# Performance work log

Measured on AMD Instinct MI355X. Metric: run time of the kernel, lower is better.

The kernel has to match this reference:

```python
import jax, jax.numpy as jnp
import numpy as np

LAMB = 0.5  # penalty coefficient (init kwarg lamb)


def setup_inputs() -> dict:
    key = jax.random.key(0)
    k1, k2, k3 = jax.random.split(key, 3)
    B, T, D, K = 4, 512, 256, 512
    reps = jax.random.normal(k1, (B, T, D), jnp.float32)
    rep_table = jax.random.normal(k2, (B, T, T, D), jnp.float32)
    centers = jax.random.normal(k3, (K, D), jnp.float32)
    return {"reps": reps, "rep_table": rep_table, "centers": centers, "timestep": T}


def reference(reps, rep_table, centers, timestep):
    B, T, D = reps.shape
    t = timestep  # min(max_len, timestep) with max_len=1e9
    dtype = reps.dtype

    # ~mask after torch.flip: row i keeps columns j >= t-1-i  (segment length i+1)
    keep = (jnp.arange(t)[None, :] >= (t - 1 - jnp.arange(t))[:, None]).astype(dtype)
    seg_lengths = jnp.arange(t, dtype=dtype) + 1.0  # (t,)

    # masked segment sum over dim 2, then average: (B, t, D)
    x = jnp.einsum('ij,bijd->bid', keep, rep_table[:, :t, :t]) / seg_lengths[None, :, None]

    # codebook attention: softmax(x C^T / sqrt(D)) C  -> (B, t, D)
    scale = 1.0 / jnp.sqrt(jnp.asarray(D, dtype))
    attn = jax.nn.softmax(jnp.einsum('bid,kd->bik', x, centers) * scale, axis=-1)
    xa = jnp.einsum('bik,kd->bid', attn, centers)

    # L2 distance to each center, expanded form to avoid (B,t,K,D) tensor
    l2 = (jnp.sum(xa * xa, axis=-1)[:, :, None]
          - 2.0 * jnp.einsum('bid,kd->bik', xa, centers)
          + jnp.sum(centers * centers, axis=-1)[None, None, :])  # (B, t, K)

    loss = l2 + (LAMB * (1.0 - seg_lengths))[None, :, None]

    val = jnp.min(loss, axis=2)      # (B, t)
    idxs = jnp.argmin(loss, axis=2)  # (B, t)

    costs = jnp.full((B, T + 1), jnp.inf, dtype).at[:, :t].set(val[:, ::-1])
    tokens = jnp.zeros((B, T + 1), jnp.int32).at[:, :t].set(idxs[:, ::-1].astype(jnp.int32))
    return costs, tokens
```

## Files before the change

kernel.cpp:

```cpp
#include <hip/hip_runtime.h>
#include <math.h>
#include <float.h>

#define TT 512
#define DD 256
#define KK 512
#define LAMBDA 0.5f

typedef float f4 __attribute__((ext_vector_type(4)));

__device__ __forceinline__ f4 ntload(const f4* p) {
    return __builtin_nontemporal_load(p);
}

__device__ __forceinline__ void fma4(f4& a, float s, f4 c) {
    a.x = fmaf(s, c.x, a.x);
    a.y = fmaf(s, c.y, a.y);
    a.z = fmaf(s, c.z, a.z);
    a.w = fmaf(s, c.w, a.w);
}

__device__ __forceinline__ unsigned short f2bf(float f) {
    unsigned int u = __float_as_uint(f);
    unsigned int r = (u + 0x7FFFu + ((u >> 16) & 1u)) >> 16;
    return (unsigned short)r;
}

__global__ __launch_bounds__(256) void seg_mean_kernel(const float* __restrict__ tbl,
                                                       float* __restrict__ x) {
    const int blk = blockIdx.x;
    const int b = blk >> 8;
    const int p = blk & 255;
    const int i0 = p;
    const int i1 = TT - 1 - p;
    const int tid = threadIdx.x;
    const int jj = tid >> 6;
    const int d4 = tid & 63;

    const f4* __restrict__ base0 =
        (const f4*)tbl + (size_t)(b * TT + i0) * (TT * (DD / 4));
    const f4* __restrict__ base1 =
        (const f4*)tbl + (size_t)(b * TT + i1) * (TT * (DD / 4));

    f4 accA = (f4)(0.f), accB = (f4)(0.f);
    {
        int j = TT - 1 - p + jj;
        for (; j + 4 < TT; j += 8) {
            f4 v0 = ntload(base0 + (size_t)j * 64 + d4);
            f4 v1 = ntload(base0 + (size_t)(j + 4) * 64 + d4);
            accA += v0; accB += v1;
        }
        if (j < TT) accA += ntload(base0 + (size_t)j * 64 + d4);
    }
    f4 acc0 = accA + accB;
    accA = (f4)(0.f); accB = (f4)(0.f);
    {
        int j = p + jj;
        for (; j + 4 < TT; j += 8) {
            f4 v0 = ntload(base1 + (size_t)j * 64 + d4);
            f4 v1 = ntload(base1 + (size_t)(j + 4) * 64 + d4);
            accA += v0; accB += v1;
        }
        if (j < TT) accA += ntload(base1 + (size_t)j * 64 + d4);
    }
    f4 acc1 = accA + accB;

    __shared__ f4 red0[4][64];
    __shared__ f4 red1[4][64];
    red0[jj][d4] = acc0;
    red1[jj][d4] = acc1;
    __syncthreads();
    if (tid < 128) {
        const int r = tid >> 6;
        const int d = tid & 63;
        const f4 (*red)[64] = r ? red1 : red0;
        const int i = r ? i1 : i0;
        f4 o = (red[0][d] + red[1][d]) + (red[2][d] + red[3][d]);
        o *= 0.0625f / (float)(i + 1);
        ((f4*)(x + (size_t)(b * TT + i) * DD))[d] = o;
    }
}

__global__ __launch_bounds__(256) void prep_kernel(const float* __restrict__ C,
                                                   float* __restrict__ CT,
                                                   float* __restrict__ cn2) {
    const int blk = blockIdx.x;
    const int tid = threadIdx.x;
    if (blk < 32) {
        __shared__ float tile[64][65];
        const int k0 = (blk & 7) * 64;
        const int d0 = (blk >> 3) * 64;
        const int kk = tid >> 4;
        const int dl = (tid & 15) * 4;
#pragma unroll
        for (int r = 0; r < 4; ++r) {
            const float4 v = *(const float4*)&C[(size_t)(k0 + kk + r * 16) * DD + d0 + dl];
            tile[kk + r * 16][dl + 0] = v.x;
            tile[kk + r * 16][dl + 1] = v.y;
            tile[kk + r * 16][dl + 2] = v.z;
            tile[kk + r * 16][dl + 3] = v.w;
        }
        __syncthreads();
        const int dd = tid >> 4;
        const int kl = (tid & 15) * 4;
#pragma unroll
        for (int r = 0; r < 4; ++r) {
            const int d = dd + r * 16;
            float4 o = make_float4(tile[kl + 0][d], tile[kl + 1][d],
                                   tile[kl + 2][d], tile[kl + 3][d]);
            *(float4*)&CT[(size_t)(d0 + d) * KK + k0 + kl] = o;
        }
    } else {
        const int w = tid >> 6, lane = tid & 63;
        const int k = (blk - 32) * 4 + w;
        const float4 v = *(const float4*)&C[(size_t)k * DD + lane * 4];
        float s = v.x * v.x + v.y * v.y + v.z * v.z + v.w * v.w;
#pragma unroll
        for (int off = 32; off > 0; off >>= 1) s += __shfl_xor(s, off, 64);
        if (lane == 0) cn2[k] = s;
    }
}

__global__ __launch_bounds__(512) void attn_argmin_kernel(
        const float* __restrict__ x, const float* __restrict__ C,
        const float* __restrict__ CT, const float* __restrict__ cn2,
        unsigned short* __restrict__ out, int Btot) {
    __shared__ char part_raw[65536];
    f4 (*scpart)[8][128] = (f4 (*)[8][128])part_raw;
    f4 (*xpart)[8][64]   = (f4 (*)[8][64])part_raw;
    __shared__ float xs[8][DD];
    __shared__ float sc[8][KK];
    __shared__ float xav[8][DD];
    __shared__ float rinv[8];
    __shared__ float xn2s[8];

    const int tid = threadIdx.x;
    const int lane = tid & 63;
    const int wv = tid >> 6;
    const int row0 = blockIdx.x * 8;

    ((f4*)&xs[0][0])[tid] = ((const f4*)(x + (size_t)row0 * DD))[tid];
    __syncthreads();

    {
        const int g = tid >> 7;
        const int k4 = tid & 127;
        const f4* CTv = (const f4*)CT + (size_t)(g * 64) * (KK / 4) + k4;
        f4 acc[8];
#pragma unroll
        for (int r = 0; r < 8; ++r) acc[r] = (f4)(0.f);
        for (int dd = 0; dd < 64; ++dd) {
            f4 c = CTv[dd * (KK / 4)];
            const int d = g * 64 + dd;
#pragma unroll
            for (int r = 0; r < 8; ++r) fma4(acc[r], xs[r][d], c);
        }
#pragma unroll
        for (int r = 0; r < 8; ++r) scpart[g][r][k4] = acc[r];
    }
    __syncthreads();
    {
#pragma unroll
        for (int it = 0; it < 2; ++it) {
            const int idx = tid * 2 + it;
            const int row = idx >> 7, k4 = idx & 127;
            f4 s = (scpart[0][row][k4] + scpart[1][row][k4])
                 + (scpart[2][row][k4] + scpart[3][row][k4]);
            ((f4*)sc[row])[k4] = s;
        }
    }
    __syncthreads();

    {
        const int r = wv;
        float v[8];
        float m = -INFINITY;
#pragma unroll
        for (int q = 0; q < 8; ++q) {
            v[q] = sc[r][lane + 64 * q];
            m = fmaxf(m, v[q]);
        }
#pragma unroll
        for (int off = 32; off > 0; off >>= 1) m = fmaxf(m, __shfl_xor(m, off, 64));
        float ssum = 0.f;
#pragma unroll
        for (int q = 0; q < 8; ++q) {
            float e = expf(v[q] - m);
            sc[r][lane + 64 * q] = e;
            ssum += e;
        }
#pragma unroll
        for (int off = 32; off > 0; off >>= 1) ssum += __shfl_xor(ssum, off, 64);
        if (lane == 0) rinv[r] = 1.f / ssum;
    }
    __syncthreads();

    {
        const int kb = wv * 64;
        const f4* Cv = (const f4*)C + (size_t)kb * (DD / 4) + lane;
        f4 acc[8];
#pragma unroll
        for (int r = 0; r < 8; ++r) acc[r] = (f4)(0.f);
        for (int kk = 0; kk < 64; ++kk) {
            f4 c = Cv[kk * (DD / 4)];
            const int k = kb + kk;
#pragma unroll
            for (int r = 0; r < 8; ++r) fma4(acc[r], sc[r][k], c);
        }
#pragma unroll
        for (int r = 0; r < 8; ++r) xpart[wv][r][lane] = acc[r];
    }
    __syncthreads();
    {
        const int row = wv, d4 = lane;
        f4 s = ((xpart[0][row][d4] + xpart[1][row][d4])
              + (xpart[2][row][d4] + xpart[3][row][d4]))
             + ((xpart[4][row][d4] + xpart[5][row][d4])
              + (xpart[6][row][d4] + xpart[7][row][d4]));
        s *= rinv[row];
        ((f4*)xav[row])[d4] = s;
        float n = s.x * s.x + s.y * s.y + s.z * s.z + s.w * s.w;
#pragma unroll
        for (int off = 32; off > 0; off >>= 1) n += __shfl_xor(n, off, 64);
        if (lane == 0) xn2s[row] = n;
    }
    __syncthreads();

    {
        const int g = tid >> 7;
        const int k4 = tid & 127;
        const f4* CTv = (const f4*)CT + (size_t)(g * 64) * (KK / 4) + k4;
        f4 acc[8];
#pragma unroll
        for (int r = 0; r < 8; ++r) acc[r] = (f4)(0.f);
        for (int dd = 0; dd < 64; ++dd) {
            f4 c = CTv[dd * (KK / 4)];
            const int d = g * 64 + dd;
#pragma unroll
            for (int r = 0; r < 8; ++r) fma4(acc[r], xav[r][d], c);
        }
#pragma unroll
        for (int r = 0; r < 8; ++r) scpart[g][r][k4] = acc[r];
    }
    __syncthreads();
    {
        float mv = FLT_MAX;
        int mi = 0;
#pragma unroll
        for (int it = 0; it < 2; ++it) {
            const int idx = tid * 2 + it;
            const int k4 = idx & 127;
            f4 dot = (scpart[0][wv][k4] + scpart[1][wv][k4])
                   + (scpart[2][wv][k4] + scpart[3][wv][k4]);
            f4 cn = ((const f4*)cn2)[k4];
            float l0 = cn.x - 2.f * dot.x;
            float l1 = cn.y - 2.f * dot.y;
            float l2 = cn.z - 2.f * dot.z;
            float l3 = cn.w - 2.f * dot.w;
            float lv = l0; int li = k4 * 4;
            if (l1 < lv) { lv = l1; li = k4 * 4 + 1; }
            if (l2 < lv) { lv = l2; li = k4 * 4 + 2; }
            if (l3 < lv) { lv = l3; li = k4 * 4 + 3; }
            if (lv < mv || (lv == mv && li < mi)) { mv = lv; mi = li; }
        }
#pragma unroll
        for (int off = 32; off > 0; off >>= 1) {
            float ov = __shfl_xor(mv, off, 64);
            int oi = __shfl_xor(mi, off, 64);
            if (ov < mv || (ov == mv && oi < mi)) { mv = ov; mi = oi; }
        }
        if (lane == 0) {
            const int row = row0 + wv;
            const int b = row >> 9;
            const int i = row & (TT - 1);
            const float pen = LAMBDA * (1.f - (float)(i + 1));
            const float val = mv + xn2s[wv] + pen;
            out[b * (TT + 1) + (TT - 1 - i)] = f2bf(val);
            out[Btot * (TT + 1) + b * (TT + 1) + (TT - 1 - i)] = f2bf((float)mi);
        }
    }
    if (tid == 511 && (row0 & (TT - 1)) == 0) {
        const int b = row0 >> 9;
        out[b * (TT + 1) + TT] = 0x7F7F;
        out[Btot * (TT + 1) + b * (TT + 1) + TT] = 0;
    }
}

extern "C" void kernel_launch(void* const* d_in, const int* in_sizes, int n_in,
                              void* d_out, int out_size, void* d_ws, size_t ws_size,
                              hipStream_t stream) {
    const float* rep_table = (const float*)d_in[1];
    const float* centers   = (const float*)d_in[2];
    unsigned short* out = (unsigned short*)d_out;

    const int Btot = in_sizes[0] / (TT * DD);

    float* x   = (float*)d_ws;
    float* CT  = x + (size_t)Btot * TT * DD;
    float* cn2 = CT + (size_t)DD * KK;

    prep_kernel<<<160, 256, 0, stream>>>(centers, CT, cn2);
    seg_mean_kernel<<<Btot * (TT / 2), 256, 0, stream>>>(rep_table, x);
    attn_argmin_kernel<<<(Btot * TT) / 8, 512, 0, stream>>>(x, centers, CT, cn2,
                                                            out, Btot);
}
```

Baseline: 113.0 us.

## Merge prep and segment-mean kernels, deepen load unroll, vectorize LDS operand reads

Folds the centers transpose/norm prep into the segment-mean launch as extra blocks, which removes one kernel launch and lets the small prep work overlap the bandwidth-bound table reduction. The segment-sum loop now keeps four independent accumulators with four loads in flight instead of two. The three small matmul loops in the attention kernel read four LDS scalars at once as one f4 and issue four global loads per step, cutting LDS instruction count. Block index ranges are hardcoded for B=4 (1024 segment blocks), so other batch sizes would break.

```diff
diff --git a/kernel.cpp b/kernel.cpp
--- a/kernel.cpp
+++ b/kernel.cpp
@@ -26,70 +26,72 @@
     return (unsigned short)r;
 }
 
-__global__ __launch_bounds__(256) void seg_mean_kernel(const float* __restrict__ tbl,
-                                                       float* __restrict__ x) {
-    const int blk = blockIdx.x;
-    const int b = blk >> 8;
-    const int p = blk & 255;
-    const int i0 = p;
-    const int i1 = TT - 1 - p;
-    const int tid = threadIdx.x;
-    const int jj = tid >> 6;
-    const int d4 = tid & 63;
-
-    const f4* __restrict__ base0 =
-        (const f4*)tbl + (size_t)(b * TT + i0) * (TT * (DD / 4));
-    const f4* __restrict__ base1 =
-        (const f4*)tbl + (size_t)(b * TT + i1) * (TT * (DD / 4));
-
-    f4 accA = (f4)(0.f), accB = (f4)(0.f);
-    {
-        int j = TT - 1 - p + jj;
-        for (; j + 4 < TT; j += 8) {
-            f4 v0 = ntload(base0 + (size_t)j * 64 + d4);
-            f4 v1 = ntload(base0 + (size_t)(j + 4) * 64 + d4);
-            accA += v0; accB += v1;
-        }
-        if (j < TT) accA += ntload(base0 + (size_t)j * 64 + d4);
-    }
-    f4 acc0 = accA + accB;
-    accA = (f4)(0.f); accB = (f4)(0.f);
-    {
-        int j = p + jj;
-        for (; j + 4 < TT; j += 8) {
-            f4 v0 = ntload(base1 + (size_t)j * 64 + d4);
-            f4 v1 = ntload(base1 + (size_t)(j + 4) * 64 + d4);
-            accA += v0; accB += v1;
-        }
-        if (j < TT) accA += ntload(base1 + (size_t)j * 64 + d4);
-    }
-    f4 acc1 = accA + accB;
-
-    __shared__ f4 red0[4][64];
-    __shared__ f4 red1[4][64];
-    red0[jj][d4] = acc0;
-    red1[jj][d4] = acc1;
-    __syncthreads();
-    if (tid < 128) {
-        const int r = tid >> 6;
-        const int d = tid & 63;
-        const f4 (*red)[64] = r ? red1 : red0;
-        const int i = r ? i1 : i0;
-        f4 o = (red[0][d] + red[1][d]) + (red[2][d] + red[3][d]);
-        o *= 0.0625f / (float)(i + 1);
-        ((f4*)(x + (size_t)(b * TT + i) * DD))[d] = o;
-    }
-}
-
-__global__ __launch_bounds__(256) void prep_kernel(const float* __restrict__ C,
-                                                   float* __restrict__ CT,
-                                                   float* __restrict__ cn2) {
+__global__ __launch_bounds__(256) void combo_kernel(
+        const float* __restrict__ tbl, const float* __restrict__ C,
+        float* __restrict__ x, float* __restrict__ CT,
+        float* __restrict__ cn2) {
     const int blk = blockIdx.x;
     const int tid = threadIdx.x;
-    if (blk < 32) {
+
+    if (blk < 1024) {
+        const int b = blk >> 8;
+        const int p = blk & 255;
+        const int i0 = p;
+        const int i1 = TT - 1 - p;
+        const int jj = tid >> 6;
+        const int d4 = tid & 63;
+
+        const f4* __restrict__ base0 =
+            (const f4*)tbl + (size_t)(b * TT + i0) * (TT * (DD / 4));
+        const f4* __restrict__ base1 =
+            (const f4*)tbl + (size_t)(b * TT + i1) * (TT * (DD / 4));
+
+        f4 a0 = (f4)(0.f), a1 = (f4)(0.f), a2 = (f4)(0.f), a3 = (f4)(0.f);
+        {
+            int j = TT - 1 - p + jj;
+            for (; j + 12 < TT; j += 16) {
+                f4 v0 = ntload(base0 + (size_t)(j + 0) * 64 + d4);
+                f4 v1 = ntload(base0 + (size_t)(j + 4) * 64 + d4);
+                f4 v2 = ntload(base0 + (size_t)(j + 8) * 64 + d4);
+                f4 v3 = ntload(base0 + (size_t)(j + 12) * 64 + d4);
+                a0 += v0; a1 += v1; a2 += v2; a3 += v3;
+            }
+            for (; j < TT; j += 4) a0 += ntload(base0 + (size_t)j * 64 + d4);
+        }
+        f4 acc0 = (a0 + a1) + (a2 + a3);
+        a0 = (f4)(0.f); a1 = (f4)(0.f); a2 = (f4)(0.f); a3 = (f4)(0.f);
+        {
+            int j = p + jj;
+            for (; j + 12 < TT; j += 16) {
+                f4 v0 = ntload(base1 + (size_t)(j + 0) * 64 + d4);
+                f4 v1 = ntload(base1 + (size_t)(j + 4) * 64 + d4);
+                f4 v2 = ntload(base1 + (size_t)(j + 8) * 64 + d4);
+                f4 v3 = ntload(base1 + (size_t)(j + 12) * 64 + d4);
+                a0 += v0; a1 += v1; a2 += v2; a3 += v3;
+            }
+            for (; j < TT; j += 4) a0 += ntload(base1 + (size_t)j * 64 + d4);
+        }
+        f4 acc1 = (a0 + a1) + (a2 + a3);
+
+        __shared__ f4 red0[4][64];
+        __shared__ f4 red1[4][64];
+        red0[jj][d4] = acc0;
+        red1[jj][d4] = acc1;
+        __syncthreads();
+        if (tid < 128) {
+            const int r = tid >> 6;
+            const int d = tid & 63;
+            const f4 (*red)[64] = r ? red1 : red0;
+            const int i = r ? i1 : i0;
+            f4 o = (red[0][d] + red[1][d]) + (red[2][d] + red[3][d]);
+            o *= 0.0625f / (float)(i + 1);
+            ((f4*)(x + (size_t)(b * TT + i) * DD))[d] = o;
+        }
+    } else if (blk < 1056) {
         __shared__ float tile[64][65];
-        const int k0 = (blk & 7) * 64;
-        const int d0 = (blk >> 3) * 64;
+        const int tb = blk - 1024;
+        const int k0 = (tb & 7) * 64;
+        const int d0 = (tb >> 3) * 64;
         const int kk = tid >> 4;
         const int dl = (tid & 15) * 4;
 #pragma unroll
@@ -112,7 +114,7 @@
         }
     } else {
         const int w = tid >> 6, lane = tid & 63;
-        const int k = (blk - 32) * 4 + w;
+        const int k = (blk - 1056) * 4 + w;
         const float4 v = *(const float4*)&C[(size_t)k * DD + lane * 4];
         float s = v.x * v.x + v.y * v.y + v.z * v.z + v.w * v.w;
 #pragma unroll
@@ -149,11 +151,19 @@
         f4 acc[8];
 #pragma unroll
         for (int r = 0; r < 8; ++r) acc[r] = (f4)(0.f);
-        for (int dd = 0; dd < 64; ++dd) {
-            f4 c = CTv[dd * (KK / 4)];
-            const int d = g * 64 + dd;
-#pragma unroll
-            for (int r = 0; r < 8; ++r) fma4(acc[r], xs[r][d], c);
+        for (int t4 = 0; t4 < 16; ++t4) {
+            f4 c0 = CTv[(t4 * 4 + 0) * (KK / 4)];
+            f4 c1 = CTv[(t4 * 4 + 1) * (KK / 4)];
+            f4 c2 = CTv[(t4 * 4 + 2) * (KK / 4)];
+            f4 c3 = CTv[(t4 * 4 + 3) * (KK / 4)];
+#pragma unroll
+            for (int r = 0; r < 8; ++r) {
+                f4 xv = ((const f4*)xs[r])[g * 16 + t4];
+                fma4(acc[r], xv.x, c0);
+                fma4(acc[r], xv.y, c1);
+                fma4(acc[r], xv.z, c2);
+                fma4(acc[r], xv.w, c3);
+            }
         }
 #pragma unroll
         for (int r = 0; r < 8; ++r) scpart[g][r][k4] = acc[r];
@@ -201,11 +211,19 @@
         f4 acc[8];
 #pragma unroll
         for (int r = 0; r < 8; ++r) acc[r] = (f4)(0.f);
-        for (int kk = 0; kk < 64; ++kk) {
-            f4 c = Cv[kk * (DD / 4)];
-            const int k = kb + kk;
-#pragma unroll
-            for (int r = 0; r < 8; ++r) fma4(acc[r], sc[r][k], c);
+        for (int k4i = 0; k4i < 16; ++k4i) {
+            f4 c0 = Cv[(k4i * 4 + 0) * (DD / 4)];
+            f4 c1 = Cv[(k4i * 4 + 1) * (DD / 4)];
+            f4 c2 = Cv[(k4i * 4 + 2) * (DD / 4)];
+            f4 c3 = Cv[(k4i * 4 + 3) * (DD / 4)];
+#pragma unroll
+            for (int r = 0; r < 8; ++r) {
+                f4 ev = ((const f4*)sc[r])[wv * 16 + k4i];
+                fma4(acc[r], ev.x, c0);
+                fma4(acc[r], ev.y, c1);
+                fma4(acc[r], ev.z, c2);
+                fma4(acc[r], ev.w, c3);
+            }
         }
 #pragma unroll
         for (int r = 0; r < 8; ++r) xpart[wv][r][lane] = acc[r];
@@ -233,11 +251,19 @@
         f4 acc[8];
 #pragma unroll
         for (int r = 0; r < 8; ++r) acc[r] = (f4)(0.f);
-        for (int dd = 0; dd < 64; ++dd) {
-            f4 c = CTv[dd * (KK / 4)];
-            const int d = g * 64 + dd;
-#pragma unroll
-            for (int r = 0; r < 8; ++r) fma4(acc[r], xav[r][d], c);
+        for (int t4 = 0; t4 < 16; ++t4) {
+            f4 c0 = CTv[(t4 * 4 + 0) * (KK / 4)];
+            f4 c1 = CTv[(t4 * 4 + 1) * (KK / 4)];
+            f4 c2 = CTv[(t4 * 4 + 2) * (KK / 4)];
+            f4 c3 = CTv[(t4 * 4 + 3) * (KK / 4)];
+#pragma unroll
+            for (int r = 0; r < 8; ++r) {
+                f4 yv = ((const f4*)xav[r])[g * 16 + t4];
+                fma4(acc[r], yv.x, c0);
+                fma4(acc[r], yv.y, c1);
+                fma4(acc[r], yv.z, c2);
+                fma4(acc[r], yv.w, c3);
+            }
         }
 #pragma unroll
         for (int r = 0; r < 8; ++r) scpart[g][r][k4] = acc[r];
@@ -299,8 +325,7 @@
     float* CT  = x + (size_t)Btot * TT * DD;
     float* cn2 = CT + (size_t)DD * KK;
 
-    prep_kernel<<<160, 256, 0, stream>>>(centers, CT, cn2);
-    seg_mean_kernel<<<Btot * (TT / 2), 256, 0, stream>>>(rep_table, x);
+    combo_kernel<<<1184, 256, 0, stream>>>(rep_table, centers, x, CT, cn2);
     attn_argmin_kernel<<<(Btot * TT) / 8, 512, 0, stream>>>(x, centers, CT, cn2,
                                                             out, Btot);
 }
```

After: 111.1 us, median of 2. About the same (-1.6%).
